# Optimization experiments

Hardware: AMD Instinct MI355X
Metric: run time of the kernel (lower is better)

The kernel has to match this reference:

```python
import jax, jax.numpy as jnp
import numpy as np

B, S, H = 2, 2048, 2048
NH, NKV, D = 16, 4, 128      # heads, kv heads, head_dim
GROUPS = NH // NKV
WIN = 1024                    # sliding window
EPS = 1e-5
THETA = 10000.0
NEG = -1e9


def _rms_norm(x, w):
    # over last dim (head_dim)
    var = jnp.mean(x * x, axis=-1, keepdims=True)
    return x * jax.lax.rsqrt(var + EPS) * w


def _rotate_half(x):
    x1, x2 = jnp.split(x, 2, axis=-1)
    return jnp.concatenate([-x2, x1], axis=-1)


def _apply_rope(q, k, cos, sin):
    # q: [B,NH,S,D], k: [B,NKV,S,D], cos/sin: [B,S,D]
    c = cos[:, None, :, :]
    s = sin[:, None, :, :]
    q = q * c + _rotate_half(q) * s
    k = k * c + _rotate_half(k) * s
    return q, k


def setup_inputs() -> dict:
    key = jax.random.key(0)
    ks = jax.random.split(key, 8)
    std = 0.02
    hidden_states = jax.random.normal(ks[0], (B, S, H), dtype=jnp.float32)
    Wq = jax.random.normal(ks[1], (NH * D, H), dtype=jnp.float32) * std
    Wk = jax.random.normal(ks[2], (NKV * D, H), dtype=jnp.float32) * std
    Wv = jax.random.normal(ks[3], (NKV * D, H), dtype=jnp.float32) * std
    Wo = jax.random.normal(ks[4], (H, NH * D), dtype=jnp.float32) * std
    Wg = jax.random.normal(ks[5], (NH * D, H), dtype=jnp.float32) * std
    q_norm_w = jnp.ones((D,), dtype=jnp.float32)
    k_norm_w = jnp.ones((D,), dtype=jnp.float32)
    # RoPE tables
    inv_freq = 1.0 / (THETA ** (jnp.arange(0, D, 2, dtype=jnp.float32) / D))
    pos = jnp.arange(S, dtype=jnp.float32)
    freqs = jnp.einsum('s,d->sd', pos, inv_freq)          # [S, D/2]
    emb = jnp.concatenate([freqs, freqs], axis=-1)        # [S, D]
    cos = jnp.broadcast_to(jnp.cos(emb)[None], (B, S, D)).astype(jnp.float32)
    sin = jnp.broadcast_to(jnp.sin(emb)[None], (B, S, D)).astype(jnp.float32)
    i = jnp.arange(S)[:, None]
    j = jnp.arange(S)[None, :]
    allowed = (j <= i) & (i - j < WIN)
    attention_mask = jnp.where(allowed, 0.0, NEG).astype(jnp.float32)[None, None]  # [1,1,S,S]
    return {
        'hidden_states': hidden_states, 'cos': cos, 'sin': sin,
        'attention_mask': attention_mask,
        'Wq': Wq, 'Wk': Wk, 'Wv': Wv, 'Wo': Wo, 'Wg': Wg,
        'q_norm_w': q_norm_w, 'k_norm_w': k_norm_w,
    }


def reference(hidden_states, cos, sin, attention_mask, Wq, Wk, Wv, Wo, Wg, q_norm_w, k_norm_w):
    x = hidden_states                                  # [B,S,H]
    q = (x @ Wq.T).reshape(B, S, NH, D)
    k = (x @ Wk.T).reshape(B, S, NKV, D)
    v = (x @ Wv.T).reshape(B, S, NKV, D)
    gate = x @ Wg.T                                    # [B,S,NH*D]
    q = _rms_norm(q, q_norm_w)
    k = _rms_norm(k, k_norm_w)
    q = q.transpose(0, 2, 1, 3)                        # [B,NH,S,D]
    k = k.transpose(0, 2, 1, 3)                        # [B,NKV,S,D]
    v = v.transpose(0, 2, 1, 3)
    # local (sliding) attention layer -> RoPE applied
    q, k = _apply_rope(q, k, cos, sin)
    # GQA: repeat kv heads
    k = jnp.repeat(k, GROUPS, axis=1)                  # [B,NH,S,D]
    v = jnp.repeat(v, GROUPS, axis=1)
    scaling = D ** -0.5
    scores = jnp.einsum('bhqd,bhkd->bhqk', q, k) * scaling
    scores = scores + attention_mask                   # broadcast [1,1,S,S]
    probs = jax.nn.softmax(scores.astype(jnp.float32), axis=-1).astype(q.dtype)
    out = jnp.einsum('bhqk,bhkd->bhqd', probs, v)      # [B,NH,S,D]
    out = out.transpose(0, 2, 1, 3).reshape(B, S, NH * D)
    out = out * jax.nn.sigmoid(gate)
    return out @ Wo.T                                  # [B,S,H]
```

## Files before the change

### kernel.cpp

```cpp
#include <hip/hip_runtime.h>
#include <hip/hip_bf16.h>

#define B_    2
#define S_    2048
#define H_    2048
#define NH_   16
#define NKV_  4
#define D_    128
#define WIN_  1024

typedef __attribute__((ext_vector_type(8))) short short8;
typedef __attribute__((ext_vector_type(4))) float f32x4;

__device__ __forceinline__ void gl2lds16(const void* g, void* l) {
  __builtin_amdgcn_global_load_lds(
      (const __attribute__((address_space(1))) void*)g,
      (__attribute__((address_space(3))) void*)l, 16, 0, 0);
}

__device__ __forceinline__ unsigned short f2bf(float x) {
  union { float f; unsigned int u; } v; v.f = x;
  unsigned int r = v.u + 0x7fffu + ((v.u >> 16) & 1u);
  return (unsigned short)(r >> 16);
}
__device__ __forceinline__ float bf2f(unsigned short u) {
  union { unsigned int i; float f; } v; v.i = ((unsigned int)u) << 16; return v.f;
}

#define CVT_TOTAL 5767168L
__global__ __launch_bounds__(256) void convert_all(
    const float* __restrict__ hs, const float* __restrict__ wq,
    const float* __restrict__ wk, const float* __restrict__ wv,
    const float* __restrict__ wg, const float* __restrict__ wo,
    unsigned short* __restrict__ xb, unsigned short* __restrict__ wall,
    unsigned short* __restrict__ wob) {
  long i = (long)blockIdx.x * 256 + threadIdx.x;
  if (i >= CVT_TOTAL) return;
  const float4* src; ushort4* dst;
  if (i < 2097152)      { src = (const float4*)hs + i;                         dst = (ushort4*)xb + i; }
  else if (i < 3145728) { long j = i - 2097152; src = (const float4*)wq + j;   dst = (ushort4*)wall + j; }
  else if (i < 3407872) { long j = i - 3145728; src = (const float4*)wk + j;   dst = (ushort4*)wall + 1048576 + j; }
  else if (i < 3670016) { long j = i - 3407872; src = (const float4*)wv + j;   dst = (ushort4*)wall + 1310720 + j; }
  else if (i < 4718592) { long j = i - 3670016; src = (const float4*)wg + j;   dst = (ushort4*)wall + 1572864 + j; }
  else                  { long j = i - 4718592; src = (const float4*)wo + j;   dst = (ushort4*)wob + j; }
  float4 v = *src;
  ushort4 o; o.x = f2bf(v.x); o.y = f2bf(v.y); o.z = f2bf(v.z); o.w = f2bf(v.w);
  *dst = o;
}

template <bool OUT_BF16>
__global__ __launch_bounds__(256) void gemm_bt(
    const unsigned short* __restrict__ A,
    const unsigned short* __restrict__ Bm,
    void* __restrict__ Cv, int M, int N, int K)
{
  __shared__ unsigned short As[128 * 32];
  __shared__ unsigned short Bs[128 * 32];
  const int t = threadIdx.x;
  const int lane = t & 63, wave = t >> 6;
  const int quad = lane >> 4, rl = lane & 15;
  const int bm = blockIdx.x * 128, bn = blockIdx.y * 128;
  const int wm = (wave >> 1) * 64, wn = (wave & 1) * 64;
  const int ldsbase = (t & ~63) * 8;

  f32x4 acc[4][4];
#pragma unroll
  for (int i = 0; i < 4; i++)
#pragma unroll
    for (int j = 0; j < 4; j++) acc[i][j] = (f32x4){0.f, 0.f, 0.f, 0.f};

  for (int k0 = 0; k0 < K; k0 += 32) {
#pragma unroll
    for (int i = 0; i < 2; i++) {
      int tt = i * 256 + t;
      int row = tt >> 2;
      int cl = (tt & 3) ^ ((row >> 1) & 3);
      gl2lds16(A + (long)(bm + row) * K + k0 + cl * 8, As + i * 2048 + ldsbase);
      gl2lds16(Bm + (long)(bn + row) * K + k0 + cl * 8, Bs + i * 2048 + ldsbase);
    }
    __syncthreads();
    short8 af[4], bfr[4];
#pragma unroll
    for (int i = 0; i < 4; i++) {
      int row = wm + i * 16 + rl;
      af[i] = *(const short8*)(As + row * 32 + ((quad ^ ((row >> 1) & 3)) * 8));
    }
#pragma unroll
    for (int j = 0; j < 4; j++) {
      int row = wn + j * 16 + rl;
      bfr[j] = *(const short8*)(Bs + row * 32 + ((quad ^ ((row >> 1) & 3)) * 8));
    }
#pragma unroll
    for (int i = 0; i < 4; i++)
#pragma unroll
      for (int j = 0; j < 4; j++)
        acc[i][j] = __builtin_amdgcn_mfma_f32_16x16x32_bf16(af[i], bfr[j], acc[i][j], 0, 0, 0);
    __syncthreads();
  }
#pragma unroll
  for (int i = 0; i < 4; i++) {
    int row0 = bm + wm + i * 16 + quad * 4;
#pragma unroll
    for (int j = 0; j < 4; j++) {
      int col = bn + wn + j * 16 + rl;
#pragma unroll
      for (int r = 0; r < 4; r++) {
        if (OUT_BF16)
          ((unsigned short*)Cv)[(long)(row0 + r) * N + col] = f2bf(acc[i][j][r]);
        else
          ((float*)Cv)[(long)(row0 + r) * N + col] = acc[i][j][r];
      }
    }
  }
}

__global__ __launch_bounds__(256) void pack_norm_rope(
    const unsigned short* __restrict__ qkvg,
    const float* __restrict__ cosb, const float* __restrict__ sinb,
    const float* __restrict__ qw, const float* __restrict__ kw,
    unsigned short* __restrict__ qb, unsigned short* __restrict__ kb)
{
  int t = threadIdx.x, lane = t & 63, wave = t >> 6;
  long gw = (long)blockIdx.x * 4 + wave;
  int hu = (int)(gw % 20);
  long bs = gw / 20;
  int b = (int)(bs / S_);
  int s = (int)(bs % S_);
  const unsigned short* row = qkvg + bs * 5120;

  bool isq = hu < 16;
  const unsigned short* base = isq ? (row + hu * 128) : (row + 2048 + (hu - 16) * 128);
  float x1 = bf2f(base[lane]), x2 = bf2f(base[lane + 64]);
  float ss = x1 * x1 + x2 * x2;
#pragma unroll
  for (int m = 1; m < 64; m <<= 1) ss += __shfl_xor(ss, m, 64);
  float inv = rsqrtf(ss * (1.0f / 128.0f) + 1e-5f);
  const float* w = isq ? qw : kw;
  float n1 = x1 * inv * w[lane], n2 = x2 * inv * w[lane + 64];
  const float* cp = cosb + bs * 128;
  const float* sp = sinb + bs * 128;
  float o1 = n1 * cp[lane] - n2 * sp[lane];
  float o2 = n2 * cp[lane + 64] + n1 * sp[lane + 64];
  if (isq) {
    long o = ((long)(b * NH_ + hu) * S_ + s) * 128;
    qb[o + lane] = f2bf(o1); qb[o + lane + 64] = f2bf(o2);
  } else {
    long o = ((long)(b * NKV_ + (hu - 16)) * S_ + s) * 128;
    kb[o + lane] = f2bf(o1); kb[o + lane + 64] = f2bf(o2);
  }
}

__global__ __launch_bounds__(256) void v_transpose(
    const unsigned short* __restrict__ qkvg, unsigned short* __restrict__ vt)
{
  __shared__ unsigned short tile[64][136];
  int t = threadIdx.x;
  int blk = blockIdx.x;
  int st = blk & 31, kv = (blk >> 5) & 3, b = blk >> 7;
  int s0 = st * 64;
#pragma unroll
  for (int i = 0; i < 4; i++) {
    int idx = i * 256 + t;
    int r = idx >> 4, c = (idx & 15) * 8;
    short8 v = *(const short8*)(qkvg + (long)(b * S_ + s0 + r) * 5120 + 2560 + kv * 128 + c);
    *(short8*)(&tile[r][c]) = v;
  }
  __syncthreads();
  long vo = (long)(b * NKV_ + kv) * 128;
#pragma unroll
  for (int i = 0; i < 8; i++) {
    int idx = i * 256 + t;
    int d = idx >> 4, sc = idx & 15;
    ushort4 o;
    o.x = tile[sc * 4 + 0][d]; o.y = tile[sc * 4 + 1][d];
    o.z = tile[sc * 4 + 2][d]; o.w = tile[sc * 4 + 3][d];
    *(ushort4*)(vt + (vo + d) * S_ + s0 + sc * 4) = o;
  }
}

#define KSTR 136
#define VSTR 72
__global__ __launch_bounds__(512, 2) void attn_kernel(
    const unsigned short* __restrict__ qb,
    const unsigned short* __restrict__ kbuf,
    const unsigned short* __restrict__ vt,
    const unsigned short* __restrict__ qkvg,
    unsigned short* __restrict__ aout)
{
  __shared__ unsigned short Ks[64 * KSTR];
  __shared__ unsigned short Vs[128 * VSTR];
  __shared__ unsigned short Ps[8][2][16 * VSTR];
  int t = threadIdx.x, lane = t & 63, wave = t >> 6;
  int quad = lane >> 4, rl = lane & 15;
  int blk = blockIdx.x;
  int qt = 31 - (blk & 31);
  int kv = (blk >> 5) & 3, b = blk >> 7;
  int h = kv * 4 + (wave >> 1);
  int half = wave & 1;
  int q0 = qt * 64;

  const unsigned short* qhead = qb + (((long)(b * NH_ + h)) * S_) * 128;
  short8 qf[2][4];
#pragma unroll
  for (int mt = 0; mt < 2; mt++)
#pragma unroll
    for (int ks = 0; ks < 4; ks++)
      qf[mt][ks] = *(const short8*)(qhead +
          (long)(q0 + half * 32 + mt * 16 + rl) * 128 + ks * 32 + quad * 8);

  f32x4 oacc[2][8];
#pragma unroll
  for (int mt = 0; mt < 2; mt++)
#pragma unroll
    for (int j = 0; j < 8; j++) oacc[mt][j] = (f32x4){0.f, 0.f, 0.f, 0.f};
  float m_r[2][4], l_r[2][4];
#pragma unroll
  for (int mt = 0; mt < 2; mt++)
#pragma unroll
    for (int r = 0; r < 4; r++) { m_r[mt][r] = -1e9f; l_r[mt][r] = 0.f; }

  const unsigned short* kbase_p = kbuf + ((long)(b * NKV_ + kv)) * S_ * 128;
  const unsigned short* vbase_p = vt + ((long)(b * NKV_ + kv)) * 128 * S_;
  int t_lo = qt - 16; if (t_lo < 0) t_lo = 0;

  int kr0 = t >> 4, kc0 = (t & 15) * 8;
  int kr1 = (t + 512) >> 4, kc1 = ((t + 512) & 15) * 8;
  int vr0 = t >> 3, vc0 = (t & 7) * 8;
  int vr1 = (t + 512) >> 3, vc1 = ((t + 512) & 7) * 8;

  {
    int kb0 = t_lo * 64;
    short8 k0v = *(const short8*)(kbase_p + (long)(kb0 + kr0) * 128 + kc0);
    short8 k1v = *(const short8*)(kbase_p + (long)(kb0 + kr1) * 128 + kc1);
    short8 v0v = *(const short8*)(vbase_p + (long)vr0 * S_ + kb0 + vc0);
    short8 v1v = *(const short8*)(vbase_p + (long)vr1 * S_ + kb0 + vc1);
    *(short8*)(Ks + kr0 * KSTR + kc0) = k0v;
    *(short8*)(Ks + kr1 * KSTR + kc1) = k1v;
    *(short8*)(Vs + vr0 * VSTR + vc0) = v0v;
    *(short8*)(Vs + vr1 * VSTR + vc1) = v1v;
  }
  __syncthreads();

  const float scale = 0.08838834764831845f;
  for (int kt = t_lo; kt <= qt; ++kt) {
    int kb0 = kt * 64;
    short8 k0v, k1v, v0v, v1v;
    if (kt < qt) {
      int nb0 = kb0 + 64;
      k0v = *(const short8*)(kbase_p + (long)(nb0 + kr0) * 128 + kc0);
      k1v = *(const short8*)(kbase_p + (long)(nb0 + kr1) * 128 + kc1);
      v0v = *(const short8*)(vbase_p + (long)vr0 * S_ + nb0 + vc0);
      v1v = *(const short8*)(vbase_p + (long)vr1 * S_ + nb0 + vc1);
    }

    f32x4 sc[2][4];
#pragma unroll
    for (int nt = 0; nt < 4; nt++) {
      f32x4 c0 = (f32x4){0.f, 0.f, 0.f, 0.f};
      f32x4 c1 = (f32x4){0.f, 0.f, 0.f, 0.f};
#pragma unroll
      for (int ks = 0; ks < 4; ks++) {
        short8 bfrag = *(const short8*)(Ks + (nt * 16 + rl) * KSTR + (ks * 4 + quad) * 8);
        c0 = __builtin_amdgcn_mfma_f32_16x16x32_bf16(qf[0][ks], bfrag, c0, 0, 0, 0);
        c1 = __builtin_amdgcn_mfma_f32_16x16x32_bf16(qf[1][ks], bfrag, c1, 0, 0, 0);
      }
      sc[0][nt] = c0; sc[1][nt] = c1;
    }
#pragma unroll
    for (int mt = 0; mt < 2; mt++) {
#pragma unroll
      for (int nt = 0; nt < 4; nt++)
#pragma unroll
        for (int r = 0; r < 4; r++) {
          int i_row = q0 + half * 32 + mt * 16 + quad * 4 + r;
          int j_col = kb0 + nt * 16 + rl;
          bool ok = (j_col <= i_row) && (i_row - j_col < WIN_);
          sc[mt][nt][r] = ok ? sc[mt][nt][r] * scale : -1e9f;
        }
#pragma unroll
      for (int r = 0; r < 4; r++) {
        float mx = fmaxf(fmaxf(sc[mt][0][r], sc[mt][1][r]),
                         fmaxf(sc[mt][2][r], sc[mt][3][r]));
#pragma unroll
        for (int m = 1; m < 16; m <<= 1) mx = fmaxf(mx, __shfl_xor(mx, m, 64));
        float newm = fmaxf(m_r[mt][r], mx);
        float alpha = __expf(m_r[mt][r] - newm);
        float p0 = __expf(sc[mt][0][r] - newm), p1 = __expf(sc[mt][1][r] - newm);
        float p2 = __expf(sc[mt][2][r] - newm), p3 = __expf(sc[mt][3][r] - newm);
        float rs = p0 + p1 + p2 + p3;
#pragma unroll
        for (int m = 1; m < 16; m <<= 1) rs += __shfl_xor(rs, m, 64);
        l_r[mt][r] = l_r[mt][r] * alpha + rs;
        m_r[mt][r] = newm;
#pragma unroll
        for (int j = 0; j < 8; j++) oacc[mt][j][r] *= alpha;
        int prow = (quad * 4 + r) * VSTR;
        unsigned short* pw = &Ps[wave][mt][prow];
        pw[0 * 16 + rl] = f2bf(p0);
        pw[1 * 16 + rl] = f2bf(p1);
        pw[2 * 16 + rl] = f2bf(p2);
        pw[3 * 16 + rl] = f2bf(p3);
      }
    }
#pragma unroll
    for (int ks2 = 0; ks2 < 2; ks2++) {
      short8 af0 = *(const short8*)(&Ps[wave][0][rl * VSTR + (ks2 * 4 + quad) * 8]);
      short8 af1 = *(const short8*)(&Ps[wave][1][rl * VSTR + (ks2 * 4 + quad) * 8]);
#pragma unroll
      for (int j = 0; j < 8; j++) {
        short8 bf2 = *(const short8*)(Vs + (j * 16 + rl) * VSTR + (ks2 * 4 + quad) * 8);
        oacc[0][j] = __builtin_amdgcn_mfma_f32_16x16x32_bf16(af0, bf2, oacc[0][j], 0, 0, 0);
        oacc[1][j] = __builtin_amdgcn_mfma_f32_16x16x32_bf16(af1, bf2, oacc[1][j], 0, 0, 0);
      }
    }
    if (kt < qt) {
      __syncthreads();
      *(short8*)(Ks + kr0 * KSTR + kc0) = k0v;
      *(short8*)(Ks + kr1 * KSTR + kc1) = k1v;
      *(short8*)(Vs + vr0 * VSTR + vc0) = v0v;
      *(short8*)(Vs + vr1 * VSTR + vc1) = v1v;
      __syncthreads();
    }
  }

#pragma unroll
  for (int mt = 0; mt < 2; mt++)
#pragma unroll
    for (int r = 0; r < 4; r++) {
      int s_idx = q0 + half * 32 + mt * 16 + quad * 4 + r;
      float invl = 1.0f / l_r[mt][r];
      long rowoff = (long)(b * S_ + s_idx);
      const unsigned short* grow = qkvg + rowoff * 5120 + 3072 + h * 128;
      unsigned short* orow = aout + rowoff * 2048 + h * 128;
#pragma unroll
      for (int j = 0; j < 8; j++) {
        int d = j * 16 + rl;
        float o = oacc[mt][j][r] * invl;
        float g = bf2f(grow[d]);
        o = o / (1.0f + __expf(-g));
        orow[d] = f2bf(o);
      }
    }
}

extern "C" void kernel_launch(void* const* d_in, const int* in_sizes, int n_in,
                              void* d_out, int out_size, void* d_ws, size_t ws_size,
                              hipStream_t stream) {
  (void)in_sizes; (void)n_in; (void)out_size; (void)ws_size;
  const float* hs   = (const float*)d_in[0];
  const float* cosb = (const float*)d_in[1];
  const float* sinb = (const float*)d_in[2];
  const float* Wq = (const float*)d_in[4];
  const float* Wk = (const float*)d_in[5];
  const float* Wv = (const float*)d_in[6];
  const float* Wo = (const float*)d_in[7];
  const float* Wg = (const float*)d_in[8];
  const float* qw = (const float*)d_in[9];
  const float* kw = (const float*)d_in[10];
  float* out = (float*)d_out;

  char* ws = (char*)d_ws;
  unsigned short* Xb   = (unsigned short*)ws; ws += (size_t)4096 * 2048 * 2;
  unsigned short* Wall = (unsigned short*)ws; ws += (size_t)5120 * 2048 * 2;
  unsigned short* Wob  = (unsigned short*)ws; ws += (size_t)2048 * 2048 * 2;
  unsigned short* qkvg = (unsigned short*)ws; ws += (size_t)4096 * 5120 * 2;
  unsigned short* qb   = (unsigned short*)ws; ws += (size_t)B_ * NH_ * S_ * D_ * 2;
  unsigned short* kbuf = (unsigned short*)ws; ws += (size_t)B_ * NKV_ * S_ * D_ * 2;
  unsigned short* vtb  = (unsigned short*)ws; ws += (size_t)B_ * NKV_ * S_ * D_ * 2;
  unsigned short* aout = (unsigned short*)ws; ws += (size_t)4096 * 2048 * 2;

  convert_all<<<(int)((CVT_TOTAL + 255) / 256), 256, 0, stream>>>(
      hs, Wq, Wk, Wv, Wg, Wo, Xb, Wall, Wob);
  gemm_bt<true><<<dim3(32, 40), 256, 0, stream>>>(Xb, Wall, (void*)qkvg, 4096, 5120, 2048);
  pack_norm_rope<<<20480, 256, 0, stream>>>(qkvg, cosb, sinb, qw, kw, qb, kbuf);
  v_transpose<<<256, 256, 0, stream>>>(qkvg, vtb);
  attn_kernel<<<256, 512, 0, stream>>>(qb, kbuf, vtb, qkvg, aout);
  gemm_bt<false><<<dim3(32, 16), 256, 0, stream>>>(aout, Wob, (void*)out, 4096, 2048, 2048);
}
```

Measured before the change: 421.0 us.

## Deepen GEMM K-tile, merge V transpose into pack kernel, split attention blocks

The GEMM now stages 64-wide K slices with a 3-bit XOR swizzle, which halves the number of barrier-separated iterations. The V transpose is folded into the norm/RoPE pack kernel as extra blocks, removing one launch. The attention kernel drops from 512-thread blocks to 256-thread blocks, one wave per head, with twice as many blocks. The goal is more scheduling flexibility, but each block now loads the K/V tiles for only 32 query rows, so K/V traffic doubles.

```diff
diff --git a/kernel.cpp b/kernel.cpp
--- a/kernel.cpp
+++ b/kernel.cpp
@@ -54,8 +54,8 @@
     const unsigned short* __restrict__ Bm,
     void* __restrict__ Cv, int M, int N, int K)
 {
-  __shared__ unsigned short As[128 * 32];
-  __shared__ unsigned short Bs[128 * 32];
+  __shared__ unsigned short As[128 * 64];
+  __shared__ unsigned short Bs[128 * 64];
   const int t = threadIdx.x;
   const int lane = t & 63, wave = t >> 6;
   const int quad = lane >> 4, rl = lane & 15;
@@ -69,32 +69,35 @@
 #pragma unroll
     for (int j = 0; j < 4; j++) acc[i][j] = (f32x4){0.f, 0.f, 0.f, 0.f};
 
-  for (int k0 = 0; k0 < K; k0 += 32) {
-#pragma unroll
-    for (int i = 0; i < 2; i++) {
+  for (int k0 = 0; k0 < K; k0 += 64) {
+#pragma unroll
+    for (int i = 0; i < 4; i++) {
       int tt = i * 256 + t;
-      int row = tt >> 2;
-      int cl = (tt & 3) ^ ((row >> 1) & 3);
-      gl2lds16(A + (long)(bm + row) * K + k0 + cl * 8, As + i * 2048 + ldsbase);
-      gl2lds16(Bm + (long)(bn + row) * K + k0 + cl * 8, Bs + i * 2048 + ldsbase);
+      int row = tt >> 3;
+      int lc = (tt & 7) ^ (row & 7);
+      gl2lds16(A + (long)(bm + row) * K + k0 + lc * 8, As + i * 2048 + ldsbase);
+      gl2lds16(Bm + (long)(bn + row) * K + k0 + lc * 8, Bs + i * 2048 + ldsbase);
     }
     __syncthreads();
-    short8 af[4], bfr[4];
-#pragma unroll
-    for (int i = 0; i < 4; i++) {
-      int row = wm + i * 16 + rl;
-      af[i] = *(const short8*)(As + row * 32 + ((quad ^ ((row >> 1) & 3)) * 8));
-    }
-#pragma unroll
-    for (int j = 0; j < 4; j++) {
-      int row = wn + j * 16 + rl;
-      bfr[j] = *(const short8*)(Bs + row * 32 + ((quad ^ ((row >> 1) & 3)) * 8));
-    }
-#pragma unroll
-    for (int i = 0; i < 4; i++)
-#pragma unroll
-      for (int j = 0; j < 4; j++)
-        acc[i][j] = __builtin_amdgcn_mfma_f32_16x16x32_bf16(af[i], bfr[j], acc[i][j], 0, 0, 0);
+#pragma unroll
+    for (int kk = 0; kk < 2; kk++) {
+      short8 af[4], bfr[4];
+#pragma unroll
+      for (int i = 0; i < 4; i++) {
+        int row = wm + i * 16 + rl;
+        af[i] = *(const short8*)(As + row * 64 + (((kk * 4 + quad) ^ (row & 7)) * 8));
+      }
+#pragma unroll
+      for (int j = 0; j < 4; j++) {
+        int row = wn + j * 16 + rl;
+        bfr[j] = *(const short8*)(Bs + row * 64 + (((kk * 4 + quad) ^ (row & 7)) * 8));
+      }
+#pragma unroll
+      for (int i = 0; i < 4; i++)
+#pragma unroll
+        for (int j = 0; j < 4; j++)
+          acc[i][j] = __builtin_amdgcn_mfma_f32_16x16x32_bf16(af[i], bfr[j], acc[i][j], 0, 0, 0);
+    }
     __syncthreads();
   }
 #pragma unroll
@@ -114,13 +117,40 @@
   }
 }
 
-__global__ __launch_bounds__(256) void pack_norm_rope(
+__global__ __launch_bounds__(256) void pack_and_transpose(
     const unsigned short* __restrict__ qkvg,
     const float* __restrict__ cosb, const float* __restrict__ sinb,
     const float* __restrict__ qw, const float* __restrict__ kw,
-    unsigned short* __restrict__ qb, unsigned short* __restrict__ kb)
+    unsigned short* __restrict__ qb, unsigned short* __restrict__ kb,
+    unsigned short* __restrict__ vt)
 {
-  int t = threadIdx.x, lane = t & 63, wave = t >> 6;
+  __shared__ unsigned short tile[64][136];
+  int t = threadIdx.x;
+  if (blockIdx.x >= 20480) {
+    int blk = blockIdx.x - 20480;
+    int st = blk & 31, kv = (blk >> 5) & 3, b = blk >> 7;
+    int s0 = st * 64;
+#pragma unroll
+    for (int i = 0; i < 4; i++) {
+      int idx = i * 256 + t;
+      int r = idx >> 4, c = (idx & 15) * 8;
+      short8 v = *(const short8*)(qkvg + (long)(b * S_ + s0 + r) * 5120 + 2560 + kv * 128 + c);
+      *(short8*)(&tile[r][c]) = v;
+    }
+    __syncthreads();
+    long vo = (long)(b * NKV_ + kv) * 128;
+#pragma unroll
+    for (int i = 0; i < 8; i++) {
+      int idx = i * 256 + t;
+      int d = idx >> 4, sc = idx & 15;
+      ushort4 o;
+      o.x = tile[sc * 4 + 0][d]; o.y = tile[sc * 4 + 1][d];
+      o.z = tile[sc * 4 + 2][d]; o.w = tile[sc * 4 + 3][d];
+      *(ushort4*)(vt + (vo + d) * S_ + s0 + sc * 4) = o;
+    }
+    return;
+  }
+  int lane = t & 63, wave = t >> 6;
   long gw = (long)blockIdx.x * 4 + wave;
   int hu = (int)(gw % 20);
   long bs = gw / 20;
@@ -150,37 +180,9 @@
   }
 }
 
-__global__ __launch_bounds__(256) void v_transpose(
-    const unsigned short* __restrict__ qkvg, unsigned short* __restrict__ vt)
-{
-  __shared__ unsigned short tile[64][136];
-  int t = threadIdx.x;
-  int blk = blockIdx.x;
-  int st = blk & 31, kv = (blk >> 5) & 3, b = blk >> 7;
-  int s0 = st * 64;
-#pragma unroll
-  for (int i = 0; i < 4; i++) {
-    int idx = i * 256 + t;
-    int r = idx >> 4, c = (idx & 15) * 8;
-    short8 v = *(const short8*)(qkvg + (long)(b * S_ + s0 + r) * 5120 + 2560 + kv * 128 + c);
-    *(short8*)(&tile[r][c]) = v;
-  }
-  __syncthreads();
-  long vo = (long)(b * NKV_ + kv) * 128;
-#pragma unroll
-  for (int i = 0; i < 8; i++) {
-    int idx = i * 256 + t;
-    int d = idx >> 4, sc = idx & 15;
-    ushort4 o;
-    o.x = tile[sc * 4 + 0][d]; o.y = tile[sc * 4 + 1][d];
-    o.z = tile[sc * 4 + 2][d]; o.w = tile[sc * 4 + 3][d];
-    *(ushort4*)(vt + (vo + d) * S_ + s0 + sc * 4) = o;
-  }
-}
-
 #define KSTR 136
 #define VSTR 72
-__global__ __launch_bounds__(512, 2) void attn_kernel(
+__global__ __launch_bounds__(256, 2) void attn_kernel(
     const unsigned short* __restrict__ qb,
     const unsigned short* __restrict__ kbuf,
     const unsigned short* __restrict__ vt,
@@ -189,14 +191,14 @@
 {
   __shared__ unsigned short Ks[64 * KSTR];
   __shared__ unsigned short Vs[128 * VSTR];
-  __shared__ unsigned short Ps[8][2][16 * VSTR];
+  __shared__ unsigned short Ps[4][2][16 * VSTR];
   int t = threadIdx.x, lane = t & 63, wave = t >> 6;
   int quad = lane >> 4, rl = lane & 15;
   int blk = blockIdx.x;
-  int qt = 31 - (blk & 31);
-  int kv = (blk >> 5) & 3, b = blk >> 7;
-  int h = kv * 4 + (wave >> 1);
-  int half = wave & 1;
+  int qh = blk & 1;
+  int qt = 31 - ((blk >> 1) & 31);
+  int kv = (blk >> 6) & 3, b = blk >> 8;
+  int h = kv * 4 + wave;
   int q0 = qt * 64;
 
   const unsigned short* qhead = qb + (((long)(b * NH_ + h)) * S_) * 128;
@@ -206,7 +208,7 @@
 #pragma unroll
     for (int ks = 0; ks < 4; ks++)
       qf[mt][ks] = *(const short8*)(qhead +
-          (long)(q0 + half * 32 + mt * 16 + rl) * 128 + ks * 32 + quad * 8);
+          (long)(q0 + qh * 32 + mt * 16 + rl) * 128 + ks * 32 + quad * 8);
 
   f32x4 oacc[2][8];
 #pragma unroll
@@ -223,34 +225,41 @@
   const unsigned short* vbase_p = vt + ((long)(b * NKV_ + kv)) * 128 * S_;
   int t_lo = qt - 16; if (t_lo < 0) t_lo = 0;
 
-  int kr0 = t >> 4, kc0 = (t & 15) * 8;
-  int kr1 = (t + 512) >> 4, kc1 = ((t + 512) & 15) * 8;
-  int vr0 = t >> 3, vc0 = (t & 7) * 8;
-  int vr1 = (t + 512) >> 3, vc1 = ((t + 512) & 7) * 8;
+  int kr[4], kc[4], vr[4], vc[4];
+#pragma unroll
+  for (int i = 0; i < 4; i++) {
+    int idx = i * 256 + t;
+    kr[i] = idx >> 4; kc[i] = (idx & 15) * 8;
+    vr[i] = idx >> 3; vc[i] = (idx & 7) * 8;
+  }
 
   {
     int kb0 = t_lo * 64;
-    short8 k0v = *(const short8*)(kbase_p + (long)(kb0 + kr0) * 128 + kc0);
-    short8 k1v = *(const short8*)(kbase_p + (long)(kb0 + kr1) * 128 + kc1);
-    short8 v0v = *(const short8*)(vbase_p + (long)vr0 * S_ + kb0 + vc0);
-    short8 v1v = *(const short8*)(vbase_p + (long)vr1 * S_ + kb0 + vc1);
-    *(short8*)(Ks + kr0 * KSTR + kc0) = k0v;
-    *(short8*)(Ks + kr1 * KSTR + kc1) = k1v;
-    *(short8*)(Vs + vr0 * VSTR + vc0) = v0v;
-    *(short8*)(Vs + vr1 * VSTR + vc1) = v1v;
+    short8 kv0[4], vv0[4];
+#pragma unroll
+    for (int i = 0; i < 4; i++) {
+      kv0[i] = *(const short8*)(kbase_p + (long)(kb0 + kr[i]) * 128 + kc[i]);
+      vv0[i] = *(const short8*)(vbase_p + (long)vr[i] * S_ + kb0 + vc[i]);
+    }
+#pragma unroll
+    for (int i = 0; i < 4; i++) {
+      *(short8*)(Ks + kr[i] * KSTR + kc[i]) = kv0[i];
+      *(short8*)(Vs + vr[i] * VSTR + vc[i]) = vv0[i];
+    }
   }
   __syncthreads();
 
   const float scale = 0.08838834764831845f;
   for (int kt = t_lo; kt <= qt; ++kt) {
     int kb0 = kt * 64;
-    short8 k0v, k1v, v0v, v1v;
+    short8 kpre[4], vpre[4];
     if (kt < qt) {
       int nb0 = kb0 + 64;
-      k0v = *(const short8*)(kbase_p + (long)(nb0 + kr0) * 128 + kc0);
-      k1v = *(const short8*)(kbase_p + (long)(nb0 + kr1) * 128 + kc1);
-      v0v = *(const short8*)(vbase_p + (long)vr0 * S_ + nb0 + vc0);
-      v1v = *(const short8*)(vbase_p + (long)vr1 * S_ + nb0 + vc1);
+#pragma unroll
+      for (int i = 0; i < 4; i++) {
+        kpre[i] = *(const short8*)(kbase_p + (long)(nb0 + kr[i]) * 128 + kc[i]);
+        vpre[i] = *(const short8*)(vbase_p + (long)vr[i] * S_ + nb0 + vc[i]);
+      }
     }
 
     f32x4 sc[2][4];
@@ -272,7 +281,7 @@
       for (int nt = 0; nt < 4; nt++)
 #pragma unroll
         for (int r = 0; r < 4; r++) {
-          int i_row = q0 + half * 32 + mt * 16 + quad * 4 + r;
+          int i_row = q0 + qh * 32 + mt * 16 + quad * 4 + r;
           int j_col = kb0 + nt * 16 + rl;
           bool ok = (j_col <= i_row) && (i_row - j_col < WIN_);
           sc[mt][nt][r] = ok ? sc[mt][nt][r] * scale : -1e9f;
@@ -315,10 +324,11 @@
     }
     if (kt < qt) {
       __syncthreads();
-      *(short8*)(Ks + kr0 * KSTR + kc0) = k0v;
-      *(short8*)(Ks + kr1 * KSTR + kc1) = k1v;
-      *(short8*)(Vs + vr0 * VSTR + vc0) = v0v;
-      *(short8*)(Vs + vr1 * VSTR + vc1) = v1v;
+#pragma unroll
+      for (int i = 0; i < 4; i++) {
+        *(short8*)(Ks + kr[i] * KSTR + kc[i]) = kpre[i];
+        *(short8*)(Vs + vr[i] * VSTR + vc[i]) = vpre[i];
+      }
       __syncthreads();
     }
   }
@@ -327,7 +337,7 @@
   for (int mt = 0; mt < 2; mt++)
 #pragma unroll
     for (int r = 0; r < 4; r++) {
-      int s_idx = q0 + half * 32 + mt * 16 + quad * 4 + r;
+      int s_idx = q0 + qh * 32 + mt * 16 + quad * 4 + r;
       float invl = 1.0f / l_r[mt][r];
       long rowoff = (long)(b * S_ + s_idx);
       const unsigned short* grow = qkvg + rowoff * 5120 + 3072 + h * 128;
@@ -372,8 +382,7 @@
   convert_all<<<(int)((CVT_TOTAL + 255) / 256), 256, 0, stream>>>(
       hs, Wq, Wk, Wv, Wg, Wo, Xb, Wall, Wob);
   gemm_bt<true><<<dim3(32, 40), 256, 0, stream>>>(Xb, Wall, (void*)qkvg, 4096, 5120, 2048);
-  pack_norm_rope<<<20480, 256, 0, stream>>>(qkvg, cosb, sinb, qw, kw, qb, kbuf);
-  v_transpose<<<256, 256, 0, stream>>>(qkvg, vtb);
-  attn_kernel<<<256, 512, 0, stream>>>(qb, kbuf, vtb, qkvg, aout);
+  pack_and_transpose<<<20736, 256, 0, stream>>>(qkvg, cosb, sinb, qw, kw, qb, kbuf, vtb);
+  attn_kernel<<<512, 256, 0, stream>>>(qb, kbuf, vtb, qkvg, aout);
   gemm_bt<false><<<dim3(32, 16), 256, 0, stream>>>(aout, Wob, (void*)out, 4096, 2048, 2048);
 }
```

Result: faster. 396.4 us (-5.9%).
